# Kernel tuning notes

Measured on AMD Instinct MI355X. Metric: run time of the kernel, lower is better.

The kernel has to match this reference:

```python
import math
import jax, jax.numpy as jnp
import numpy as np

B, S, D, P, H = 8, 512, 1024, 128, 8  # batch, seq_len, dim, phase_dim, num_heads


def _layernorm(v, g, b, eps=1e-5):
    m = jnp.mean(v, axis=-1, keepdims=True)
    var = jnp.mean((v - m) ** 2, axis=-1, keepdims=True)
    return (v - m) * jax.lax.rsqrt(var + eps) * g + b


def setup_inputs() -> dict:
    key = jax.random.key(0)
    ks = jax.random.split(key, 12)
    s = 0.02
    f32 = jnp.float32
    return {
        'x':   jax.random.normal(ks[0], (B, S, D), f32),
        'Wa':  jax.random.normal(ks[1], (D, P), f32) * s,
        'ba':  jnp.zeros((P,), f32),
        'Wp':  jax.random.normal(ks[2], (D, P), f32) * s,
        'bp':  jnp.zeros((P,), f32),
        'g1':  jnp.ones((P,), f32),
        'bt1': jnp.zeros((P,), f32),
        'W1':  jax.random.normal(ks[3], (H, P, 2 * P), f32) * s,
        'bh1': jnp.zeros((H, 2 * P), f32),
        'W2':  jax.random.normal(ks[4], (H, 2 * P, P), f32) * s,
        'bh2': jnp.zeros((H, P), f32),
        'g2':  jnp.ones((P,), f32),
        'bt2': jnp.zeros((P,), f32),
        'Wo':  jax.random.normal(ks[5], (H * P, D), f32) * s,
        'bo':  jnp.zeros((D,), f32),
    }


def reference(x, Wa, ba, Wp, bp, g1, bt1, W1, bh1, W2, bh2, g2, bt2, Wo, bo):
    # amplitude/phase encoding; only the real part is ever used downstream
    amp = jnp.tanh(x @ Wa + ba)                       # [B,S,P]
    ph = jax.nn.sigmoid(x @ Wp + bp) * (2.0 * math.pi)
    real = amp * jnp.cos(ph)                          # [B,S,P]

    xn = _layernorm(real, g1, bt1)                    # shared norm1
    # per-head MLP, vectorized over heads via einsum
    t = jax.nn.gelu(jnp.einsum('bsp,hpq->hbsq', xn, W1) + bh1[:, None, None, :],
                    approximate=False)
    t = jnp.einsum('hbsq,hqp->hbsp', t, W2) + bh2[:, None, None, :]  # [H,B,S,P]

    # per-(head,sample,channel) self cross-correlation of the transformed
    # signal with itself (the conv1d(x, x, groups=batch) trick), padding=S//2,
    # truncated to S lags so it gates elementwise.
    C = H * B * P
    Tc = jnp.transpose(t, (0, 1, 3, 2)).reshape(1, C, S)   # [1, C, S]
    w = Tc.reshape(C, 1, S)                                 # one kernel per channel
    pad = S // 2
    inter = jax.lax.conv_general_dilated(Tc, w, (1,), [(pad, pad)],
                                         feature_group_count=C)  # [1, C, S+1]
    inter = inter[0, :, :S].reshape(H, B, P, S)
    inter = jnp.transpose(inter, (0, 1, 3, 2))              # [H,B,S,P]

    gated = real[None] * jax.nn.sigmoid(inter)              # [H,B,S,P]
    comb = jnp.transpose(gated, (1, 2, 0, 3))               # [B,S,H,P]
    nrm = _layernorm(comb, g2, bt2).reshape(B, S, H * P)    # norm2 per head
    return nrm @ Wo + bo + x
```

## Files before the change

kernel.cpp:

```cpp
#include <hip/hip_runtime.h>
#include <math.h>

typedef __attribute__((ext_vector_type(8))) short bf16x8_t;
typedef __attribute__((ext_vector_type(4))) float f32x4_t;

__device__ __forceinline__ float sigmoidf_(float x){ return 1.f/(1.f+expf(-x)); }
__device__ __forceinline__ float geluf_(float x){ return 0.5f*x*(1.f+erff(x*0.70710678118654752f)); }
__device__ __forceinline__ unsigned short f2bf(float x){
  unsigned int u = __float_as_uint(x);
  return (unsigned short)((u + 0x7fffu + ((u>>16)&1u)) >> 16);
}
__device__ __forceinline__ float bf2f(unsigned short h){
  return __uint_as_float(((unsigned int)h)<<16);
}
__device__ __forceinline__ bf16x8_t ldfrag(const unsigned short* p){
  union { bf16x8_t v; uint2 q[2]; } u;
  u.q[0] = *(const uint2*)p; u.q[1] = *(const uint2*)(p+4); return u.v;
}
__device__ __forceinline__ bf16x8_t ldfrag16(const unsigned short* p){
  union { bf16x8_t v; uint4 q; } u; u.q = *(const uint4*)p; return u.v;
}

__global__ __launch_bounds__(256) void bias_pack(const float* __restrict__ ba,
    const float* __restrict__ bp, float* __restrict__ bcat){
  int t = threadIdx.x; bcat[t] = (t<128)? ba[t] : bp[t-128];
}

__global__ __launch_bounds__(256) void transpose_split(
    const float* __restrict__ src, unsigned short* __restrict__ dhi,
    unsigned short* __restrict__ dlo, int R, int C)
{
  long zoff = (long)blockIdx.z * R * C;
  src += zoff; dhi += zoff; dlo += zoff;
  __shared__ float tile[32][33];
  int c0 = blockIdx.x*32, r0 = blockIdx.y*32;
  int j = threadIdx.x & 31, i0 = threadIdx.x >> 5;
  #pragma unroll
  for (int ii=0; ii<4; ++ii){ int i = i0 + ii*8;
    tile[i][j] = src[(long)(r0+i)*C + c0 + j]; }
  __syncthreads();
  #pragma unroll
  for (int ii=0; ii<4; ++ii){ int i = i0 + ii*8;
    float v = tile[j][i];
    unsigned short h = f2bf(v);
    dhi[(long)(c0+i)*R + r0 + j] = h;
    dlo[(long)(c0+i)*R + r0 + j] = f2bf(v - bf2f(h));
  }
}

template<int EPI>
__global__ __launch_bounds__(256) void gemm_mfma(
    const float* __restrict__ A, const unsigned short* __restrict__ Bhi,
    const unsigned short* __restrict__ Blo,
    const float* __restrict__ bias, const float* __restrict__ resid,
    float* __restrict__ C, int M, int N, int K,
    long sA, long sB, long sBias, long sC)
{
  int z = blockIdx.z;
  A += (long)z*sA; Bhi += (long)z*sB; Blo += (long)z*sB; bias += (long)z*sBias; C += (long)z*sC;
  __shared__ unsigned short As_hi[64][68], As_lo[64][68];
  __shared__ unsigned short Bs_hi[128][68], Bs_lo[128][68];
  const int tid = threadIdx.x;
  const int lane = tid & 63, wv = tid >> 6;
  const int wr = wv >> 1, wc = wv & 1;
  const int mw = wr*32, nw = wc*64;
  const int la = lane & 15, kg = (lane >> 4) << 3;
  const int m0 = blockIdx.x * 64, n0 = blockIdx.y * 128;

  f32x4_t acc[2][4];
  #pragma unroll
  for (int i=0;i<2;++i)
    #pragma unroll
    for (int j=0;j<4;++j) acc[i][j] = (f32x4_t){0.f,0.f,0.f,0.f};

  for (int k0 = 0; k0 < K; k0 += 64) {
    float4 av[4]; uint4 bh4[4], bl4[4];
    #pragma unroll
    for (int r=0;r<4;++r){
      int ia = tid + r*256;
      av[r] = *(const float4*)(A + (long)(m0 + (ia>>4))*K + k0 + ((ia&15)<<2));
      int ib = tid + r*256;
      long bo = (long)(n0 + (ib>>3))*K + k0 + ((ib&7)<<3);
      bh4[r] = *(const uint4*)(Bhi + bo);
      bl4[r] = *(const uint4*)(Blo + bo);
    }
    __syncthreads();
    #pragma unroll
    for (int r=0;r<4;++r){
      int ia = tid + r*256;
      int arow = ia>>4, akc = (ia&15)<<2;
      float4 v = av[r];
      unsigned short h0=f2bf(v.x),h1=f2bf(v.y),h2=f2bf(v.z),h3=f2bf(v.w);
      uint2 whi; whi.x = (unsigned)h0 | ((unsigned)h1<<16); whi.y = (unsigned)h2 | ((unsigned)h3<<16);
      *(uint2*)&As_hi[arow][akc] = whi;
      unsigned short l0=f2bf(v.x-bf2f(h0)),l1=f2bf(v.y-bf2f(h1)),
                     l2=f2bf(v.z-bf2f(h2)),l3=f2bf(v.w-bf2f(h3));
      uint2 wlo; wlo.x = (unsigned)l0 | ((unsigned)l1<<16); wlo.y = (unsigned)l2 | ((unsigned)l3<<16);
      *(uint2*)&As_lo[arow][akc] = wlo;
      int ib = tid + r*256;
      int bn = ib>>3, bkc = (ib&7)<<3;
      uint2 t0; t0.x = bh4[r].x; t0.y = bh4[r].y;
      uint2 t1; t1.x = bh4[r].z; t1.y = bh4[r].w;
      *(uint2*)&Bs_hi[bn][bkc]   = t0;
      *(uint2*)&Bs_hi[bn][bkc+4] = t1;
      uint2 t2; t2.x = bl4[r].x; t2.y = bl4[r].y;
      uint2 t3; t3.x = bl4[r].z; t3.y = bl4[r].w;
      *(uint2*)&Bs_lo[bn][bkc]   = t2;
      *(uint2*)&Bs_lo[bn][bkc+4] = t3;
    }
    __syncthreads();
    #pragma unroll
    for (int kk=0; kk<2; ++kk){
      bf16x8_t ah[2], al[2], bh[4], bl[4];
      #pragma unroll
      for (int mf=0; mf<2; ++mf){
        ah[mf] = ldfrag(&As_hi[mw + mf*16 + la][kk*32 + kg]);
        al[mf] = ldfrag(&As_lo[mw + mf*16 + la][kk*32 + kg]);
      }
      #pragma unroll
      for (int nf=0; nf<4; ++nf){
        bh[nf] = ldfrag(&Bs_hi[nw + nf*16 + la][kk*32 + kg]);
        bl[nf] = ldfrag(&Bs_lo[nw + nf*16 + la][kk*32 + kg]);
      }
      #pragma unroll
      for (int mf=0; mf<2; ++mf)
        #pragma unroll
        for (int nf=0; nf<4; ++nf){
          acc[mf][nf] = __builtin_amdgcn_mfma_f32_16x16x32_bf16(ah[mf], bh[nf], acc[mf][nf], 0,0,0);
          acc[mf][nf] = __builtin_amdgcn_mfma_f32_16x16x32_bf16(ah[mf], bl[nf], acc[mf][nf], 0,0,0);
          acc[mf][nf] = __builtin_amdgcn_mfma_f32_16x16x32_bf16(al[mf], bh[nf], acc[mf][nf], 0,0,0);
        }
    }
  }
  #pragma unroll
  for (int mf=0; mf<2; ++mf){
    int grow0 = m0 + mw + mf*16 + ((lane>>4)<<2);
    #pragma unroll
    for (int nf=0; nf<4; ++nf){
      int gcol = n0 + nw + nf*16 + la;
      float bsv = bias[gcol];
      if (EPI==4){
        float4 o;
        o.x = acc[mf][nf][0] + bsv; o.y = acc[mf][nf][1] + bsv;
        o.z = acc[mf][nf][2] + bsv; o.w = acc[mf][nf][3] + bsv;
        *(float4*)(C + (long)gcol*M + grow0) = o;
      } else {
        #pragma unroll
        for (int r=0;r<4;++r){
          int grow = grow0 + r;
          float v = acc[mf][nf][r] + bsv;
          if (EPI==1) v = geluf_(v);
          if (EPI==2) v += resid[(long)grow*N + gcol];
          C[(long)grow*N + gcol] = v;
        }
      }
    }
  }
}

__global__ __launch_bounds__(256) void encode_ln_kernel(
    const float* __restrict__ E, const float* __restrict__ g1, const float* __restrict__ bt1,
    float* __restrict__ realp, float* __restrict__ xnp)
{
  int wv = threadIdx.x >> 6, lane = threadIdx.x & 63;
  long row = (long)blockIdx.x*4 + wv;
  const float* e = E + row*256;
  int p = lane*2;
  float2 a = *(const float2*)(e + p);
  float2 f = *(const float2*)(e + 128 + p);
  const float TWO_PI = 6.28318530717958647692f;
  float r0 = tanhf(a.x) * cosf(TWO_PI * sigmoidf_(f.x));
  float r1 = tanhf(a.y) * cosf(TWO_PI * sigmoidf_(f.y));
  float s = r0+r1, ss = r0*r0 + r1*r1;
  #pragma unroll
  for (int m=1;m<64;m<<=1){ s += __shfl_xor(s,m,64); ss += __shfl_xor(ss,m,64); }
  float mean = s * (1.f/128.f);
  float var  = ss * (1.f/128.f) - mean*mean;
  float inv  = rsqrtf(var + 1e-5f);
  float x0 = (r0-mean)*inv*g1[p]   + bt1[p];
  float x1 = (r1-mean)*inv*g1[p+1] + bt1[p+1];
  *(float2*)(realp + row*128 + p) = make_float2(r0,r1);
  *(float2*)(xnp   + row*128 + p) = make_float2(x0,x1);
}

__device__ __forceinline__ int hi_off_(int d){ return d ? (512 + d*1280) : 0; }
__device__ __forceinline__ int lo_off_(int d){ return d ? (1152 + d*1280) : 896; }
__device__ __forceinline__ int physpad_(int m){ return m + ((m >> 6) << 3); }

__global__ __launch_bounds__(256) void autocorr_kernel(
    const float* __restrict__ tT, float* __restrict__ sig)
{
  __shared__ __align__(16) unsigned short pool[4][5632];
  const int tid = threadIdx.x;
  const int wv = tid >> 6, lane = tid & 63;
  int bidx = blockIdx.x;
  int p4 = bidx & 31; int hb = bidx >> 5; int b = hb & 7, h = hb >> 3;

  unsigned int* pz = (unsigned int*)&pool[0][0];
  for (int i = tid; i < 4*5632/2; i += 256) pz[i] = 0u;
  __syncthreads();

  unsigned short* P = pool[wv];
  {
    const float* tp = tT + ((long)(h*128 + p4*4 + wv))*4096 + b*512;
    for (int i = lane; i < 512; i += 64) {
      float v = tp[i];
      unsigned short hh = f2bf(v);
      unsigned short ll = f2bf(v - bf2f(hh));
      #pragma unroll
      for (int d = 0; d < 4; ++d) {
        int ph = physpad_(i + 16 - d);
        P[hi_off_(d) + ph] = hh;
        P[lo_off_(d) + ph] = ll;
      }
    }
  }
  __syncthreads();

  const int la = lane & 15, kg8 = (lane >> 4) << 3;
  f32x4_t acc = (f32x4_t){0.f,0.f,0.f,0.f};
  for (int kb = 0; kb < 17; ++kb) {
    int qA = kb*32 + kg8 + la*16 + 16;
    int phA = physpad_(qA);
    bf16x8_t Ah = ldfrag16(P + phA);
    bf16x8_t Al = ldfrag16(P + 896 + phA);
    int qB = kb*32 + kg8 + 16 - la;
    int d = qB & 3;
    int r0 = qB - d, r1 = r0 + 4;
    int ph0 = physpad_(r0), ph1 = physpad_(r1);
    int hio = hi_off_(d), loo = lo_off_(d);
    union { bf16x8_t v; uint2 q[2]; } ub, vb;
    ub.q[0] = *(const uint2*)(P + hio + ph0);
    ub.q[1] = *(const uint2*)(P + hio + ph1);
    vb.q[0] = *(const uint2*)(P + loo + ph0);
    vb.q[1] = *(const uint2*)(P + loo + ph1);
    acc = __builtin_amdgcn_mfma_f32_16x16x32_bf16(Ah, ub.v, acc, 0,0,0);
    acc = __builtin_amdgcn_mfma_f32_16x16x32_bf16(Ah, vb.v, acc, 0,0,0);
    acc = __builtin_amdgcn_mfma_f32_16x16x32_bf16(Al, ub.v, acc, 0,0,0);
  }

  float r256 = 0.f;
  #pragma unroll
  for (int u = 0; u < 4; ++u) {
    int t = lane*4 + u;
    int p1 = physpad_(t + 16), p2 = physpad_(t + 272);
    float v1 = bf2f(P[p1]) + bf2f(P[896 + p1]);
    float v2 = bf2f(P[p2]) + bf2f(P[896 + p2]);
    r256 = fmaf(v1, v2, r256);
  }
  #pragma unroll
  for (int m = 1; m < 64; m <<= 1) r256 += __shfl_xor(r256, m, 64);

  float* sp = sig + ((long)(h*4096 + b*512))*128 + p4*4 + wv;
  int arow = (lane >> 4) << 2;
  #pragma unroll
  for (int rr = 0; rr < 4; ++rr) {
    int lam = (arow + rr)*16 + la;
    float bv = sigmoidf_(acc[rr]);
    sp[(long)(256+lam)*128] = bv;
    if (lam > 0) sp[(long)(256-lam)*128] = bv;
  }
  if (lane == 0) sp[0] = sigmoidf_(r256);
}

__global__ __launch_bounds__(256) void gate_ln_kernel(
    const float* __restrict__ realp, const float* __restrict__ sig,
    const float* __restrict__ g2, const float* __restrict__ bt2,
    float* __restrict__ y)
{
  int wv = threadIdx.x >> 6, lane = threadIdx.x & 63;
  long r = (long)blockIdx.x*4 + wv;
  int h = (int)(r >> 12);
  long rem = r & 4095;
  int p = lane*2;
  float2 rv = *(const float2*)(realp + rem*128 + p);
  float2 sv = *(const float2*)(sig + r*128 + p);
  float a0 = rv.x*sv.x, a1 = rv.y*sv.y;
  float s = a0+a1, ss = a0*a0+a1*a1;
  #pragma unroll
  for (int m=1;m<64;m<<=1){ s += __shfl_xor(s,m,64); ss += __shfl_xor(ss,m,64); }
  float mean = s*(1.f/128.f);
  float var  = ss*(1.f/128.f) - mean*mean;
  float inv  = rsqrtf(var+1e-5f);
  float y0 = (a0-mean)*inv*g2[p]   + bt2[p];
  float y1 = (a1-mean)*inv*g2[p+1] + bt2[p+1];
  *(float2*)(y + rem*1024 + h*128 + p) = make_float2(y0,y1);
}

extern "C" void kernel_launch(void* const* d_in, const int* in_sizes, int n_in,
                              void* d_out, int out_size, void* d_ws, size_t ws_size,
                              hipStream_t stream)
{
  const float* x   = (const float*)d_in[0];
  const float* Wa  = (const float*)d_in[1];
  const float* ba  = (const float*)d_in[2];
  const float* Wp  = (const float*)d_in[3];
  const float* bp  = (const float*)d_in[4];
  const float* g1  = (const float*)d_in[5];
  const float* bt1 = (const float*)d_in[6];
  const float* W1  = (const float*)d_in[7];
  const float* bh1 = (const float*)d_in[8];
  const float* W2  = (const float*)d_in[9];
  const float* bh2 = (const float*)d_in[10];
  const float* g2  = (const float*)d_in[11];
  const float* bt2 = (const float*)d_in[12];
  const float* Wo  = (const float*)d_in[13];
  const float* bo  = (const float*)d_in[14];

  char* p = (char*)d_ws;
  auto alloc = [&](size_t bytes)->char*{ char* r = p; p += (bytes + 255) & ~(size_t)255; return r; };
  float* bcat = (float*)alloc(256*4);
  unsigned short* WcatT_hi = (unsigned short*)alloc(256*1024*2);
  unsigned short* WcatT_lo = (unsigned short*)alloc(256*1024*2);
  unsigned short* W1T_hi   = (unsigned short*)alloc(8*256*128*2);
  unsigned short* W1T_lo   = (unsigned short*)alloc(8*256*128*2);
  unsigned short* W2T_hi   = (unsigned short*)alloc(8*128*256*2);
  unsigned short* W2T_lo   = (unsigned short*)alloc(8*128*256*2);
  unsigned short* WoT_hi   = (unsigned short*)alloc(1024*1024*2);
  unsigned short* WoT_lo   = (unsigned short*)alloc(1024*1024*2);
  float* E     = (float*)alloc((size_t)4096*256*4);
  float* realp = (float*)alloc((size_t)4096*128*4);
  float* xnp   = (float*)alloc((size_t)4096*128*4);
  float* hid   = (float*)alloc((size_t)8*4096*256*4);
  float* tbuf  = (float*)alloc((size_t)8*128*4096*4);
  float* sigb  = hid;
  float* ybuf  = tbuf;
  float* out   = (float*)d_out;

  bias_pack<<<1,256,0,stream>>>(ba,bp,bcat);
  transpose_split<<<dim3(4,32,1),256,0,stream>>>(Wa, WcatT_hi, WcatT_lo, 1024,128);
  transpose_split<<<dim3(4,32,1),256,0,stream>>>(Wp, WcatT_hi+131072, WcatT_lo+131072, 1024,128);
  transpose_split<<<dim3(8,4,8),256,0,stream>>>(W1, W1T_hi, W1T_lo, 128,256);
  transpose_split<<<dim3(4,8,8),256,0,stream>>>(W2, W2T_hi, W2T_lo, 256,128);
  transpose_split<<<dim3(32,32,1),256,0,stream>>>(Wo, WoT_hi, WoT_lo, 1024,1024);

  gemm_mfma<0><<<dim3(64,2,1),256,0,stream>>>(x, WcatT_hi, WcatT_lo, bcat, nullptr, E,
                                              4096,256,1024, 0,0,0,0);
  encode_ln_kernel<<<1024,256,0,stream>>>(E,g1,bt1,realp,xnp);
  gemm_mfma<1><<<dim3(64,2,8),256,0,stream>>>(xnp, W1T_hi, W1T_lo, bh1, nullptr, hid,
                                              4096,256,128, 0, (long)256*128, 256, (long)4096*256);
  gemm_mfma<4><<<dim3(64,1,8),256,0,stream>>>(hid, W2T_hi, W2T_lo, bh2, nullptr, tbuf,
                                              4096,128,256, (long)4096*256, (long)128*256, 128, (long)128*4096);
  autocorr_kernel<<<2048,256,0,stream>>>(tbuf, sigb);
  gate_ln_kernel<<<8192,256,0,stream>>>(realp, sigb, g2, bt2, ybuf);
  gemm_mfma<2><<<dim3(64,8,1),256,0,stream>>>(ybuf, WoT_hi, WoT_lo, bo, x, out,
                                              4096,1024,1024, 0,0,0,0);
}
```

Measured before the change: 257.6 us.

## Use single-bf16 output GEMM and stage autocorr gate writes through LDS

Replaces the final output projection with a new 64x64-tiled MFMA kernel that rounds activations and Wo to a single bf16 term, dropping the hi/lo split-precision products. This cuts MFMA work and removes the lo-weight reads for the largest GEMM, but lowers accuracy of that projection. The autocorrelation kernel now stages per-wave sigmoid results in shared memory and writes them as float4 vectors across four channels, replacing strided scalar global stores.

```diff
diff --git a/kernel.cpp b/kernel.cpp
--- a/kernel.cpp
+++ b/kernel.cpp
@@ -150,9 +150,90 @@
           int grow = grow0 + r;
           float v = acc[mf][nf][r] + bsv;
           if (EPI==1) v = geluf_(v);
-          if (EPI==2) v += resid[(long)grow*N + gcol];
           C[(long)grow*N + gcol] = v;
         }
+      }
+    }
+  }
+}
+
+__global__ __launch_bounds__(256) void gemm_out_kernel(
+    const float* __restrict__ A, const unsigned short* __restrict__ Bhi,
+    const float* __restrict__ bias, const float* __restrict__ resid,
+    float* __restrict__ C, int M, int N, int K)
+{
+  __shared__ unsigned short As[64][68];
+  __shared__ unsigned short Bs[64][68];
+  const int tid = threadIdx.x;
+  const int lane = tid & 63, wv = tid >> 6;
+  const int wr = wv >> 1, wc = wv & 1;
+  const int mw = wr*32, nw = wc*32;
+  const int la = lane & 15, kg = (lane >> 4) << 3;
+  const int m0 = blockIdx.x * 64, n0 = blockIdx.y * 64;
+
+  f32x4_t acc[2][2];
+  #pragma unroll
+  for (int i=0;i<2;++i)
+    #pragma unroll
+    for (int j=0;j<2;++j) acc[i][j] = (f32x4_t){0.f,0.f,0.f,0.f};
+
+  for (int k0 = 0; k0 < K; k0 += 64) {
+    float4 av[4]; uint4 b4[2];
+    #pragma unroll
+    for (int r=0;r<4;++r){
+      int ia = tid + r*256;
+      av[r] = *(const float4*)(A + (long)(m0 + (ia>>4))*K + k0 + ((ia&15)<<2));
+    }
+    #pragma unroll
+    for (int r=0;r<2;++r){
+      int ib = tid + r*256;
+      b4[r] = *(const uint4*)(Bhi + (long)(n0 + (ib>>3))*K + k0 + ((ib&7)<<3));
+    }
+    __syncthreads();
+    #pragma unroll
+    for (int r=0;r<4;++r){
+      int ia = tid + r*256;
+      int arow = ia>>4, akc = (ia&15)<<2;
+      float4 v = av[r];
+      unsigned short h0=f2bf(v.x),h1=f2bf(v.y),h2=f2bf(v.z),h3=f2bf(v.w);
+      uint2 w; w.x = (unsigned)h0 | ((unsigned)h1<<16); w.y = (unsigned)h2 | ((unsigned)h3<<16);
+      *(uint2*)&As[arow][akc] = w;
+    }
+    #pragma unroll
+    for (int r=0;r<2;++r){
+      int ib = tid + r*256;
+      int brow = ib>>3, bkc = (ib&7)<<3;
+      uint2 t0; t0.x = b4[r].x; t0.y = b4[r].y;
+      uint2 t1; t1.x = b4[r].z; t1.y = b4[r].w;
+      *(uint2*)&Bs[brow][bkc]   = t0;
+      *(uint2*)&Bs[brow][bkc+4] = t1;
+    }
+    __syncthreads();
+    #pragma unroll
+    for (int kk=0; kk<2; ++kk){
+      bf16x8_t a[2], b[2];
+      #pragma unroll
+      for (int mf=0; mf<2; ++mf) a[mf] = ldfrag(&As[mw + mf*16 + la][kk*32 + kg]);
+      #pragma unroll
+      for (int nf=0; nf<2; ++nf) b[nf] = ldfrag(&Bs[nw + nf*16 + la][kk*32 + kg]);
+      #pragma unroll
+      for (int mf=0; mf<2; ++mf)
+        #pragma unroll
+        for (int nf=0; nf<2; ++nf)
+          acc[mf][nf] = __builtin_amdgcn_mfma_f32_16x16x32_bf16(a[mf], b[nf], acc[mf][nf], 0,0,0);
+    }
+  }
+  #pragma unroll
+  for (int mf=0; mf<2; ++mf){
+    int grow0 = m0 + mw + mf*16 + ((lane>>4)<<2);
+    #pragma unroll
+    for (int nf=0; nf<2; ++nf){
+      int gcol = n0 + nw + nf*16 + la;
+      float bsv = bias[gcol];
+      #pragma unroll
+      for (int r=0;r<4;++r){
+        int grow = grow0 + r;
+        C[(long)grow*N + gcol] = acc[mf][nf][r] + bsv + resid[(long)grow*N + gcol];
       }
     }
   }
@@ -191,6 +272,7 @@
     const float* __restrict__ tT, float* __restrict__ sig)
 {
   __shared__ __align__(16) unsigned short pool[4][5632];
+  __shared__ float sbuf[4][516];
   const int tid = threadIdx.x;
   const int wv = tid >> 6, lane = tid & 63;
   int bidx = blockIdx.x;
@@ -251,16 +333,24 @@
   #pragma unroll
   for (int m = 1; m < 64; m <<= 1) r256 += __shfl_xor(r256, m, 64);
 
-  float* sp = sig + ((long)(h*4096 + b*512))*128 + p4*4 + wv;
+  float* SB = sbuf[wv];
   int arow = (lane >> 4) << 2;
   #pragma unroll
   for (int rr = 0; rr < 4; ++rr) {
     int lam = (arow + rr)*16 + la;
     float bv = sigmoidf_(acc[rr]);
-    sp[(long)(256+lam)*128] = bv;
-    if (lam > 0) sp[(long)(256-lam)*128] = bv;
-  }
-  if (lane == 0) sp[0] = sigmoidf_(r256);
+    SB[256+lam] = bv;
+    if (lam > 0) SB[256-lam] = bv;
+  }
+  if (lane == 0) SB[0] = sigmoidf_(r256);
+  __syncthreads();
+
+  float* outp = sig + ((long)(h*4096 + b*512))*128 + p4*4;
+  for (int s = tid; s < 512; s += 256) {
+    float4 o;
+    o.x = sbuf[0][s]; o.y = sbuf[1][s]; o.z = sbuf[2][s]; o.w = sbuf[3][s];
+    *(float4*)(outp + (long)s*128) = o;
+  }
 }
 
 __global__ __launch_bounds__(256) void gate_ln_kernel(
@@ -343,6 +433,6 @@
                                               4096,128,256, (long)4096*256, (long)128*256, 128, (long)128*4096);
   autocorr_kernel<<<2048,256,0,stream>>>(tbuf, sigb);
   gate_ln_kernel<<<8192,256,0,stream>>>(realp, sigb, g2, bt2, ybuf);
-  gemm_mfma<2><<<dim3(64,8,1),256,0,stream>>>(ybuf, WoT_hi, WoT_lo, bo, x, out,
-                                              4096,1024,1024, 0,0,0,0);
-}
+  gemm_out_kernel<<<dim3(64,16,1),256,0,stream>>>(ybuf, WoT_hi, bo, x, out,
+                                                  4096,1024,1024);
+}
```

Result: faster. 250.9 us (-2.6%).
